# Performance work log

Measured on AMD Instinct MI355X. Metric: run time of the kernel, lower is better.

## Reference

```python
import jax, jax.numpy as jnp
import numpy as np

D_MODEL = 1024
N_HEADS = 16
D_K = D_MODEL // N_HEADS


def setup_inputs() -> dict:
    key = jax.random.key(0)
    ks = jax.random.split(key, 12)
    B, S = 4, 2048
    sc = 1.0 / np.sqrt(D_MODEL)
    inp = {
        "query": jax.random.normal(ks[0], (B, S, D_MODEL), jnp.float32),
        "key": jax.random.normal(ks[1], (B, S, D_MODEL), jnp.float32),
        "value": jax.random.normal(ks[2], (B, S, D_MODEL), jnp.float32),
        "Wq": jax.random.normal(ks[3], (D_MODEL, D_MODEL), jnp.float32) * sc,
        "bq": jnp.zeros((D_MODEL,), jnp.float32),
        "Wk": jax.random.normal(ks[4], (D_MODEL, D_MODEL), jnp.float32) * sc,
        "bk": jnp.zeros((D_MODEL,), jnp.float32),
        "Wv": jax.random.normal(ks[5], (D_MODEL, D_MODEL), jnp.float32) * sc,
        "bv": jnp.zeros((D_MODEL,), jnp.float32),
        "Wo": jax.random.normal(ks[6], (D_MODEL, D_MODEL), jnp.float32) * sc,
        "bo": jnp.zeros((D_MODEL,), jnp.float32),
    }
    return inp


def _split_heads(x):
    B, S, _ = x.shape
    return x.reshape(B, S, N_HEADS, D_K).transpose(0, 2, 1, 3)  # [B,H,S,Dk]


def reference(query, key, value, Wq, bq, Wk, bk, Wv, bv, Wo, bo):
    q = _split_heads(query @ Wq.T + bq)
    k = _split_heads(key @ Wk.T + bk)
    v = _split_heads(value @ Wv.T + bv)
    scores = jnp.einsum("bhqd,bhkd->bhqk", q, k) / jnp.sqrt(jnp.float32(D_K))
    # Faithful to source: softmax over dim=1 (the HEAD axis), a quirk of the original.
    probs = jax.nn.softmax(scores, axis=1)
    attn = jnp.einsum("bhqk,bhkd->bhqd", probs, v)
    B, H, S, Dk = attn.shape
    combined = attn.transpose(0, 2, 1, 3).reshape(B, S, H * Dk)
    return combined @ Wo.T + bo
```

## Files before the change

### kernel.cpp

```cpp
#include <hip/hip_runtime.h>
#include <stdint.h>

typedef __attribute__((ext_vector_type(8))) short bf16x8;
typedef __attribute__((ext_vector_type(4))) float f32x4;
typedef __attribute__((ext_vector_type(4))) float fl4;
typedef __attribute__((ext_vector_type(4))) unsigned short u16x4;
typedef __attribute__((ext_vector_type(8))) unsigned short u16x8;

constexpr int SEQ = 2048;
constexpr int DMODEL = 1024;
constexpr int NH = 16;
constexpr int DKH = 64;
constexpr float SEXP = 0.18033688f;

__device__ __forceinline__ unsigned short f2bf(float x) {
  union { float f; uint32_t u; } c;
  c.f = x;
  uint32_t u = c.u;
  u += 0x7FFFu + ((u >> 16) & 1u);
  return (unsigned short)(u >> 16);
}

__device__ __forceinline__ float bf2f(unsigned short u) {
  union { uint32_t u; float f; } c;
  c.u = ((uint32_t)u) << 16;
  return c.f;
}

__device__ __forceinline__ uint32_t cvtpk(float lo, float hi) {
  uint32_t r;
  asm("v_cvt_pk_bf16_f32 %0, %1, %2" : "=v"(r) : "v"(lo), "v"(hi));
  return r;
}

#if __has_builtin(__builtin_amdgcn_exp2f)
__device__ __forceinline__ float fexp2(float x) { return __builtin_amdgcn_exp2f(x); }
#else
__device__ __forceinline__ float fexp2(float x) { return exp2f(x); }
#endif

__device__ __forceinline__ int swz(int row) { return (row & 3) ^ ((row >> 2) & 3); }

__device__ __forceinline__ void gload16(const unsigned short* g, unsigned short* l) {
  __builtin_amdgcn_global_load_lds((const __attribute__((address_space(1))) void*)g,
                                   (__attribute__((address_space(3))) void*)l, 16, 0, 0);
}

__global__ __launch_bounds__(256) void cvtk(
    const float* __restrict__ s0, const float* __restrict__ s1, const float* __restrict__ s2,
    unsigned short* __restrict__ d0, unsigned short* __restrict__ d1, unsigned short* __restrict__ d2) {
  const float* s = blockIdx.y == 0 ? s0 : blockIdx.y == 1 ? s1 : s2;
  unsigned short* d = blockIdx.y == 0 ? d0 : blockIdx.y == 1 ? d1 : d2;
  const size_t i = ((size_t)blockIdx.x * 256 + threadIdx.x) * 8;
  fl4 a = *(const fl4*)(s + i);
  fl4 c = *(const fl4*)(s + i + 4);
  u16x8 r;
#pragma unroll
  for (int j = 0; j < 4; ++j) { r[j] = f2bf(a[j]); r[4 + j] = f2bf(c[j]); }
  *(u16x8*)(d + i) = r;
}

__global__ __launch_bounds__(256) void cvt1(
    const float* __restrict__ s, unsigned short* __restrict__ d) {
  const size_t i = ((size_t)blockIdx.x * 256 + threadIdx.x) * 8;
  fl4 a = *(const fl4*)(s + i);
  fl4 c = *(const fl4*)(s + i + 4);
  u16x8 r;
#pragma unroll
  for (int j = 0; j < 4; ++j) { r[j] = f2bf(a[j]); r[4 + j] = f2bf(c[j]); }
  *(u16x8*)(d + i) = r;
}

__global__ __launch_bounds__(256, 2) void gemmqkv(
    const float* __restrict__ Xq, const float* __restrict__ Xk, const float* __restrict__ Xv,
    const unsigned short* __restrict__ Wb,
    const float* __restrict__ bq, const float* __restrict__ bk, const float* __restrict__ bv,
    unsigned short* __restrict__ Qp, unsigned short* __restrict__ Kp, unsigned short* __restrict__ Vt) {
  constexpr int K = DMODEL;
  __shared__ unsigned short As[2][128 * 32];
  __shared__ unsigned short Bs[2][128 * 32];
  const int tid = threadIdx.x;
  const int wave = tid >> 6, lane = tid & 63;
  const int g = lane >> 4, ln = lane & 15;
  const int o = blockIdx.x;
  const int x = o & 7, j = o >> 3;
  const int si = j >> 5, w = j & 31;
  const int seg = si >> 1;
  const int r0 = (x * 8 + (si & 1) * 4 + (w & 3)) * 128;
  const int c0 = (w >> 2) * 128;
  const int wr = (wave >> 1) * 64, wc = (wave & 1) * 64;
  const int arow = tid >> 2, cc = tid & 3;

  const float* A = seg == 0 ? Xq : seg == 1 ? Xk : Xv;
  const unsigned short* Bw = Wb + (size_t)seg * DMODEL * DMODEL;
  const float* bias = seg == 0 ? bq : seg == 1 ? bk : bv;
  const float ascale = seg == 0 ? SEXP : 1.0f;

  f32x4 acc[4][4] = {};
  fl4 ar[2][2];

  auto LOADA = [&](int kt) {
#pragma unroll
    for (int i = 0; i < 2; ++i) {
      const size_t ao = (size_t)(r0 + arow + i * 64) * K + kt + cc * 8;
      ar[i][0] = *(const fl4*)(A + ao);
      ar[i][1] = *(const fl4*)(A + ao + 4);
    }
  };
  auto WRITEA = [&](int buf) {
#pragma unroll
    for (int i = 0; i < 2; ++i) {
      const int row = arow + i * 64;
      const int ch = (cc ^ swz(row)) * 8;
      union { uint32_t u[4]; u16x8 v; } pk;
      pk.u[0] = cvtpk(ar[i][0][0], ar[i][0][1]);
      pk.u[1] = cvtpk(ar[i][0][2], ar[i][0][3]);
      pk.u[2] = cvtpk(ar[i][1][0], ar[i][1][1]);
      pk.u[3] = cvtpk(ar[i][1][2], ar[i][1][3]);
      *(u16x8*)(As[buf] + row * 32 + ch) = pk.v;
    }
  };
  auto STAGEB = [&](int buf, int kt) {
#pragma unroll
    for (int i = 0; i < 2; ++i) {
      const int row = i * 64 + (tid >> 2);
      const int cs = ((tid & 3) ^ swz(row)) * 8;
      gload16(Bw + (size_t)(c0 + row) * K + kt + cs, Bs[buf] + (i * 256 + wave * 64) * 8);
    }
  };

  LOADA(0);
  WRITEA(0);
  STAGEB(0, 0);
  __syncthreads();

  for (int t = 0; t < K / 32; ++t) {
    const int buf = t & 1;
    if (t + 1 < K / 32) { LOADA((t + 1) * 32); STAGEB(buf ^ 1, (t + 1) * 32); }
    bf16x8 af[4], bfr[4];
#pragma unroll
    for (int m = 0; m < 4; ++m) {
      const int row = wr + m * 16 + ln;
      af[m] = *(const bf16x8*)(As[buf] + row * 32 + ((g ^ swz(row)) * 8));
    }
#pragma unroll
    for (int n = 0; n < 4; ++n) {
      const int row = wc + n * 16 + ln;
      bfr[n] = *(const bf16x8*)(Bs[buf] + row * 32 + ((g ^ swz(row)) * 8));
    }
#pragma unroll
    for (int m = 0; m < 4; ++m)
#pragma unroll
      for (int n = 0; n < 4; ++n)
        acc[m][n] = __builtin_amdgcn_mfma_f32_16x16x32_bf16(af[m], bfr[n], acc[m][n], 0, 0, 0);
    if (t + 1 < K / 32) WRITEA(buf ^ 1);
    __syncthreads();
  }

#pragma unroll
  for (int m = 0; m < 4; ++m) {
    const int row = r0 + wr + m * 16 + g * 4;
#pragma unroll
    for (int n = 0; n < 4; ++n) {
      const int col = c0 + wc + n * 16 + ln;
      const float bvv = bias[col];
      f32x4 v = acc[m][n];
      if (seg < 2) {
        unsigned short* C = seg == 0 ? Qp : Kp;
#pragma unroll
        for (int r = 0; r < 4; ++r) C[(size_t)(row + r) * DMODEL + col] = f2bf((v[r] + bvv) * ascale);
      } else {
        const int bb = row >> 11, sl = row & 2047;
        const int h = col >> 6, d = col & 63;
        const int sp = (sl & ~31) | (((sl >> 2) & 3) << 3) | (((sl >> 4) & 1) << 2);
        u16x4 pk;
#pragma unroll
        for (int r = 0; r < 4; ++r) pk[r] = f2bf(v[r] + bvv);
        *(u16x4*)(Vt + ((size_t)((bb * NH + h) * DKH + d)) * SEQ + sp) = pk;
      }
    }
  }
}

__global__ __launch_bounds__(256, 2) void gemmout(
    const unsigned short* __restrict__ A, const unsigned short* __restrict__ Bb,
    const float* __restrict__ bias, float* __restrict__ Cp) {
  constexpr int K = DMODEL;
  constexpr int N = DMODEL;
  __shared__ unsigned short As[2][128 * 32];
  __shared__ unsigned short Bs[2][128 * 32];
  const int tid = threadIdx.x;
  const int wave = tid >> 6, lane = tid & 63;
  const int g = lane >> 4, ln = lane & 15;
  const int o = blockIdx.x;
  const int x = o & 7, idx = o >> 3;
  const int r0 = (x * 8 + (idx & 7)) * 128;
  const int c0 = (idx >> 3) * 128;
  const int wr = (wave >> 1) * 64, wc = (wave & 1) * 64;

  f32x4 acc[4][4] = {};

  auto STAGE = [&](int buf, int kt) {
#pragma unroll
    for (int i = 0; i < 2; ++i) {
      const int row = i * 64 + (tid >> 2);
      const int cs = ((tid & 3) ^ swz(row)) * 8;
      gload16(A + (size_t)(r0 + row) * K + kt + cs, As[buf] + (i * 256 + wave * 64) * 8);
      gload16(Bb + (size_t)(c0 + row) * K + kt + cs, Bs[buf] + (i * 256 + wave * 64) * 8);
    }
  };

  STAGE(0, 0);
  __syncthreads();

  for (int t = 0; t < K / 32; ++t) {
    const int buf = t & 1;
    if (t + 1 < K / 32) STAGE(buf ^ 1, (t + 1) * 32);
    bf16x8 af[4], bfr[4];
#pragma unroll
    for (int m = 0; m < 4; ++m) {
      const int row = wr + m * 16 + ln;
      af[m] = *(const bf16x8*)(As[buf] + row * 32 + ((g ^ swz(row)) * 8));
    }
#pragma unroll
    for (int n = 0; n < 4; ++n) {
      const int row = wc + n * 16 + ln;
      bfr[n] = *(const bf16x8*)(Bs[buf] + row * 32 + ((g ^ swz(row)) * 8));
    }
#pragma unroll
    for (int m = 0; m < 4; ++m)
#pragma unroll
      for (int n = 0; n < 4; ++n)
        acc[m][n] = __builtin_amdgcn_mfma_f32_16x16x32_bf16(af[m], bfr[n], acc[m][n], 0, 0, 0);
    __syncthreads();
  }

#pragma unroll
  for (int m = 0; m < 4; ++m) {
    const int row = r0 + wr + m * 16 + g * 4;
#pragma unroll
    for (int n = 0; n < 4; ++n) {
      const int col = c0 + wc + n * 16 + ln;
      const float bvv = bias[col];
      f32x4 v = acc[m][n];
#pragma unroll
      for (int r = 0; r < 4; ++r) Cp[(size_t)(row + r) * N + col] = v[r] + bvv;
    }
  }
}

__global__ __launch_bounds__(256, 3) void denomk(
    const unsigned short* __restrict__ Qp, const unsigned short* __restrict__ Kp,
    unsigned short* __restrict__ rDb) {
  __shared__ unsigned short Ks[2][128 * 64];
  const int tid = threadIdx.x, wave = tid >> 6, lane = tid & 63;
  const int g = lane >> 4, ln = lane & 15;
  const int o = blockIdx.x;
  const int l = (o & 7) * 256 + (o >> 3);
  const int b = l >> 9;
  const int qg = (l >> 4) & 31;
  const int kvg = l & 15;
  const int q0 = qg * 64, kvb = kvg * 128;
  const int kw = wave * 32;

  auto STAGE = [&](int buf, int h) {
#pragma unroll
    for (int i = 0; i < 4; ++i) {
      const int s = i * 256 + tid;
      const int row = s >> 3, c = s & 7;
      gload16(Kp + (size_t)(b * SEQ + kvb + row) * DMODEL + h * DKH + ((c ^ (row & 7)) * 8),
              Ks[buf] + (i * 256 + wave * 64) * 8);
    }
  };

  f32x4 psum[2][4] = {};

  STAGE(0, 0);
  __syncthreads();

  for (int h = 0; h < NH; ++h) {
    const int buf = h & 1;
    if (h + 1 < NH) STAGE(buf ^ 1, h + 1);
    bf16x8 qf[2][4];
#pragma unroll
    for (int ks = 0; ks < 2; ++ks)
#pragma unroll
      for (int n = 0; n < 4; ++n)
        qf[ks][n] = *(const bf16x8*)(Qp + (size_t)(b * SEQ + q0 + n * 16 + ln) * DMODEL + h * DKH + ks * 32 + g * 8);
    bf16x8 kf[2][2];
#pragma unroll
    for (int m = 0; m < 2; ++m)
#pragma unroll
      for (int ks = 0; ks < 2; ++ks) {
        const int r = kw + m * 16 + ln;
        const int cc = ks * 4 + g;
        kf[m][ks] = *(const bf16x8*)(Ks[buf] + r * 64 + ((cc ^ (r & 7)) * 8));
      }
    f32x4 s[2][4] = {};
#pragma unroll
    for (int m = 0; m < 2; ++m)
#pragma unroll
      for (int n = 0; n < 4; ++n) {
        s[m][n] = __builtin_amdgcn_mfma_f32_16x16x32_bf16(kf[m][0], qf[0][n], s[m][n], 0, 0, 0);
        s[m][n] = __builtin_amdgcn_mfma_f32_16x16x32_bf16(kf[m][1], qf[1][n], s[m][n], 0, 0, 0);
      }
#pragma unroll
    for (int m = 0; m < 2; ++m)
#pragma unroll
      for (int n = 0; n < 4; ++n)
#pragma unroll
        for (int r = 0; r < 4; ++r) psum[m][n][r] += fexp2(s[m][n][r]);
    __syncthreads();
  }

#pragma unroll
  for (int m = 0; m < 2; ++m)
#pragma unroll
    for (int n = 0; n < 4; ++n) {
      u16x4 st;
#pragma unroll
      for (int r = 0; r < 4; ++r) st[r] = f2bf(1.0f / psum[m][n][r]);
      *(u16x4*)(rDb + (size_t)(b * SEQ + q0 + n * 16 + ln) * SEQ + kvb + kw + m * 16 + g * 4) = st;
    }
}

__global__ __launch_bounds__(256, 4) void flashk(
    const unsigned short* __restrict__ Qp, const unsigned short* __restrict__ Kp,
    const unsigned short* __restrict__ Vt, const unsigned short* __restrict__ rDb,
    unsigned short* __restrict__ Ab) {
  __shared__ unsigned short Ks[2][64 * 64];
  __shared__ unsigned short Vs[2][64 * 64];
  const int tid = threadIdx.x, wave = tid >> 6, lane = tid & 63;
  const int g = lane >> 4, ln = lane & 15;
  const int o = blockIdx.x;
  const int l = (o & 7) * 128 + (o >> 3);
  const int b = l >> 8;
  const int h = (l >> 4) & 15;
  const int q0 = (l & 15) * 128 + wave * 32;

  bf16x8 qf[2][2];
#pragma unroll
  for (int ks = 0; ks < 2; ++ks)
#pragma unroll
    for (int n = 0; n < 2; ++n)
      qf[ks][n] = *(const bf16x8*)(Qp + (size_t)(b * SEQ + q0 + n * 16 + ln) * DMODEL + h * DKH + ks * 32 + g * 8);

  f32x4 ao[4][2] = {};
  const size_t rbase0 = (size_t)(b * SEQ + q0 + ln) * SEQ;
  const size_t kbase = (size_t)(b * SEQ) * DMODEL + h * DKH;
  const size_t vbase = (size_t)((b * NH + h) * DKH) * SEQ;

  auto STAGE = [&](int buf, int kv0) {
#pragma unroll
    for (int i = 0; i < 2; ++i) {
      const int s = i * 256 + tid;
      const int row = s >> 3, c = s & 7;
      gload16(Kp + kbase + (size_t)(kv0 + row) * DMODEL + ((c ^ (row & 7)) * 8),
              Ks[buf] + (i * 256 + wave * 64) * 8);
    }
#pragma unroll
    for (int i = 0; i < 2; ++i) {
      const int s = i * 256 + tid;
      const int row = s >> 3, c = s & 7;
      gload16(Vt + vbase + (size_t)row * SEQ + kv0 + ((c ^ (row & 7)) * 8),
              Vs[buf] + (i * 256 + wave * 64) * 8);
    }
  };

  STAGE(0, 0);
  __syncthreads();

  for (int t = 0; t < SEQ / 64; ++t) {
    const int kv0 = t * 64, buf = t & 1;
    if (t + 1 < SEQ / 64) STAGE(buf ^ 1, kv0 + 64);

#pragma unroll
    for (int si = 0; si < 2; ++si) {
      u16x4 rdq[2][2];
#pragma unroll
      for (int n = 0; n < 2; ++n)
#pragma unroll
        for (int m = 0; m < 2; ++m)
          rdq[n][m] = *(const u16x4*)(rDb + rbase0 + (size_t)(n * 16) * SEQ + kv0 + si * 32 + m * 16 + g * 4);

      f32x4 s2[2][2] = {};
      __builtin_amdgcn_s_setprio(1);
#pragma unroll
      for (int m = 0; m < 2; ++m) {
        const int row = si * 32 + m * 16 + ln;
#pragma unroll
        for (int ks = 0; ks < 2; ++ks) {
          const int cc = ks * 4 + g;
          bf16x8 kf = *(const bf16x8*)(Ks[buf] + row * 64 + ((cc ^ (row & 7)) * 8));
#pragma unroll
          for (int n = 0; n < 2; ++n)
            s2[m][n] = __builtin_amdgcn_mfma_f32_16x16x32_bf16(kf, qf[ks][n], s2[m][n], 0, 0, 0);
        }
      }
      __builtin_amdgcn_s_setprio(0);

      bf16x8 pfr[2];
#pragma unroll
      for (int n = 0; n < 2; ++n) {
        uint32_t dw[4];
#pragma unroll
        for (int m = 0; m < 2; ++m) {
          float p0 = fexp2(s2[m][n][0]) * bf2f(rdq[n][m][0]);
          float p1 = fexp2(s2[m][n][1]) * bf2f(rdq[n][m][1]);
          float p2 = fexp2(s2[m][n][2]) * bf2f(rdq[n][m][2]);
          float p3 = fexp2(s2[m][n][3]) * bf2f(rdq[n][m][3]);
          dw[m * 2 + 0] = cvtpk(p0, p1);
          dw[m * 2 + 1] = cvtpk(p2, p3);
        }
        union { uint32_t u[4]; bf16x8 v; } cv;
        cv.u[0] = dw[0]; cv.u[1] = dw[1]; cv.u[2] = dw[2]; cv.u[3] = dw[3];
        pfr[n] = cv.v;
      }

      __builtin_amdgcn_s_setprio(1);
#pragma unroll
      for (int dt = 0; dt < 4; ++dt) {
        const int vrow = dt * 16 + ln;
        const int vc = si * 4 + g;
        bf16x8 vf = *(const bf16x8*)(Vs[buf] + vrow * 64 + ((vc ^ (vrow & 7)) * 8));
#pragma unroll
        for (int n = 0; n < 2; ++n)
          ao[dt][n] = __builtin_amdgcn_mfma_f32_16x16x32_bf16(vf, pfr[n], ao[dt][n], 0, 0, 0);
      }
      __builtin_amdgcn_s_setprio(0);
    }
    __syncthreads();
  }

#pragma unroll
  for (int dt = 0; dt < 4; ++dt)
#pragma unroll
    for (int n = 0; n < 2; ++n) {
      u16x4 st;
#pragma unroll
      for (int r = 0; r < 4; ++r) st[r] = f2bf(ao[dt][n][r]);
      *(u16x4*)(Ab + (size_t)(b * SEQ + q0 + n * 16 + ln) * DMODEL + h * DKH + dt * 16 + g * 4) = st;
    }
}

extern "C" void kernel_launch(void* const* d_in, const int* in_sizes, int n_in,
                              void* d_out, int out_size, void* d_ws, size_t ws_size,
                              hipStream_t stream) {
  (void)in_sizes; (void)n_in; (void)out_size; (void)ws_size;
  const float* query = (const float*)d_in[0];
  const float* key   = (const float*)d_in[1];
  const float* value = (const float*)d_in[2];
  const float* Wq = (const float*)d_in[3];
  const float* bq = (const float*)d_in[4];
  const float* Wk = (const float*)d_in[5];
  const float* bk = (const float*)d_in[6];
  const float* Wv = (const float*)d_in[7];
  const float* bv = (const float*)d_in[8];
  const float* Wo = (const float*)d_in[9];
  const float* bo = (const float*)d_in[10];

  uint8_t* ws = (uint8_t*)d_ws;
  const size_t SZ = (size_t)4 * SEQ * DMODEL * 2;
  const size_t WSZ = (size_t)DMODEL * DMODEL;
  unsigned short* Qp  = (unsigned short*)(ws);
  unsigned short* Wob = (unsigned short*)(ws);
  unsigned short* Kp  = (unsigned short*)(ws + SZ);
  unsigned short* Vt  = (unsigned short*)(ws + 2 * SZ);
  unsigned short* Wqb = (unsigned short*)(ws + 3 * SZ);
  unsigned short* Wkb = Wqb + WSZ;
  unsigned short* Wvb = Wqb + 2 * WSZ;
  unsigned short* Ab  = (unsigned short*)(ws + 3 * SZ);
  unsigned short* rDb = (unsigned short*)d_out;

  cvtk<<<dim3(512, 3), 256, 0, stream>>>(Wq, Wk, Wv, Wqb, Wkb, Wvb);
  gemmqkv<<<1536, 256, 0, stream>>>(query, key, value, Wqb, bq, bk, bv, Qp, Kp, Vt);
  denomk<<<2048, 256, 0, stream>>>(Qp, Kp, rDb);
  flashk<<<1024, 256, 0, stream>>>(Qp, Kp, Vt, rDb, Ab);
  cvt1<<<512, 256, 0, stream>>>(Wo, Wob);
  gemmout<<<512, 256, 0, stream>>>(Ab, Wob, bo, (float*)d_out);
}
```

Measured before the change: 388.6 us.

## Replace __syncthreads with explicit vmcnt waits to keep prefetch loads in flight

All four main kernels (QKV projection, output projection, denominator, attention) replace __syncthreads with raw s_barrier plus partial s_waitcnt vmcnt counts, using sched_barrier to fix instruction order. The next tile's loads stay outstanding while the current tile is computed, removing the full memory drain that __syncthreads forces. Loop-tail prefetches are made unconditional with wrapped indices, and the attention kernel hoists both halves of the rDb loads before the barrier. The risk is hand-counted vmcnt values that must exactly match the number of issued loads, plus a redundant extra prefetch on the last iteration.

```diff
diff --git a/kernel.cpp b/kernel.cpp
--- a/kernel.cpp
+++ b/kernel.cpp
@@ -45,6 +45,11 @@
   __builtin_amdgcn_global_load_lds((const __attribute__((address_space(1))) void*)g,
                                    (__attribute__((address_space(3))) void*)l, 16, 0, 0);
 }
+
+#define SB() __builtin_amdgcn_sched_barrier(0)
+#define VW(N) do { SB(); asm volatile("s_waitcnt vmcnt(" #N ")" ::: "memory"); SB(); } while (0)
+#define LGKM0() do { SB(); asm volatile("s_waitcnt lgkmcnt(0)" ::: "memory"); SB(); } while (0)
+__device__ __forceinline__ void bar() { SB(); __builtin_amdgcn_s_barrier(); SB(); }
 
 __global__ __launch_bounds__(256) void cvtk(
     const float* __restrict__ s0, const float* __restrict__ s1, const float* __restrict__ s2,
@@ -128,34 +133,45 @@
       gload16(Bw + (size_t)(c0 + row) * K + kt + cs, Bs[buf] + (i * 256 + wave * 64) * 8);
     }
   };
+  auto COMPUTE = [&](int buf) {
+    bf16x8 af[4], bfr[4];
+#pragma unroll
+    for (int m = 0; m < 4; ++m) {
+      const int row = wr + m * 16 + ln;
+      af[m] = *(const bf16x8*)(As[buf] + row * 32 + ((g ^ swz(row)) * 8));
+    }
+#pragma unroll
+    for (int n = 0; n < 4; ++n) {
+      const int row = wc + n * 16 + ln;
+      bfr[n] = *(const bf16x8*)(Bs[buf] + row * 32 + ((g ^ swz(row)) * 8));
+    }
+#pragma unroll
+    for (int m = 0; m < 4; ++m)
+#pragma unroll
+      for (int n = 0; n < 4; ++n)
+        acc[m][n] = __builtin_amdgcn_mfma_f32_16x16x32_bf16(af[m], bfr[n], acc[m][n], 0, 0, 0);
+  };
 
   LOADA(0);
   WRITEA(0);
   STAGEB(0, 0);
-  __syncthreads();
+  LGKM0();
+  bar();
 
   for (int t = 0; t < K / 32; ++t) {
     const int buf = t & 1;
-    if (t + 1 < K / 32) { LOADA((t + 1) * 32); STAGEB(buf ^ 1, (t + 1) * 32); }
-    bf16x8 af[4], bfr[4];
-#pragma unroll
-    for (int m = 0; m < 4; ++m) {
-      const int row = wr + m * 16 + ln;
-      af[m] = *(const bf16x8*)(As[buf] + row * 32 + ((g ^ swz(row)) * 8));
-    }
-#pragma unroll
-    for (int n = 0; n < 4; ++n) {
-      const int row = wc + n * 16 + ln;
-      bfr[n] = *(const bf16x8*)(Bs[buf] + row * 32 + ((g ^ swz(row)) * 8));
-    }
-#pragma unroll
-    for (int m = 0; m < 4; ++m)
-#pragma unroll
-      for (int n = 0; n < 4; ++n)
-        acc[m][n] = __builtin_amdgcn_mfma_f32_16x16x32_bf16(af[m], bfr[n], acc[m][n], 0, 0, 0);
-    if (t + 1 < K / 32) WRITEA(buf ^ 1);
-    __syncthreads();
+    const int ktn = ((t + 1) & 31) * 32;
+    STAGEB(buf ^ 1, ktn);
+    SB();
+    LOADA(ktn);
+    VW(6);
+    bar();
+    COMPUTE(buf);
+    WRITEA(buf ^ 1);
+    LGKM0();
+    bar();
   }
+  VW(0);
 
 #pragma unroll
   for (int m = 0; m < 4; ++m) {
@@ -211,11 +227,12 @@
   };
 
   STAGE(0, 0);
-  __syncthreads();
 
   for (int t = 0; t < K / 32; ++t) {
     const int buf = t & 1;
-    if (t + 1 < K / 32) STAGE(buf ^ 1, (t + 1) * 32);
+    STAGE(buf ^ 1, ((t + 1) & 31) * 32);
+    VW(4);
+    bar();
     bf16x8 af[4], bfr[4];
 #pragma unroll
     for (int m = 0; m < 4; ++m) {
@@ -232,8 +249,9 @@
 #pragma unroll
       for (int n = 0; n < 4; ++n)
         acc[m][n] = __builtin_amdgcn_mfma_f32_16x16x32_bf16(af[m], bfr[n], acc[m][n], 0, 0, 0);
-    __syncthreads();
+    bar();
   }
+  VW(0);
 
 #pragma unroll
   for (int m = 0; m < 4; ++m) {
@@ -276,17 +294,19 @@
   f32x4 psum[2][4] = {};
 
   STAGE(0, 0);
-  __syncthreads();
 
   for (int h = 0; h < NH; ++h) {
     const int buf = h & 1;
-    if (h + 1 < NH) STAGE(buf ^ 1, h + 1);
+    STAGE(buf ^ 1, (h + 1) & 15);
+    SB();
     bf16x8 qf[2][4];
 #pragma unroll
     for (int ks = 0; ks < 2; ++ks)
 #pragma unroll
       for (int n = 0; n < 4; ++n)
         qf[ks][n] = *(const bf16x8*)(Qp + (size_t)(b * SEQ + q0 + n * 16 + ln) * DMODEL + h * DKH + ks * 32 + g * 8);
+    VW(12);
+    bar();
     bf16x8 kf[2][2];
 #pragma unroll
     for (int m = 0; m < 2; ++m)
@@ -310,8 +330,9 @@
       for (int n = 0; n < 4; ++n)
 #pragma unroll
         for (int r = 0; r < 4; ++r) psum[m][n][r] += fexp2(s[m][n][r]);
-    __syncthreads();
+    bar();
   }
+  VW(0);
 
 #pragma unroll
   for (int m = 0; m < 2; ++m)
@@ -368,21 +389,24 @@
   };
 
   STAGE(0, 0);
-  __syncthreads();
 
   for (int t = 0; t < SEQ / 64; ++t) {
     const int kv0 = t * 64, buf = t & 1;
-    if (t + 1 < SEQ / 64) STAGE(buf ^ 1, kv0 + 64);
+    STAGE(buf ^ 1, (kv0 + 64) & (SEQ - 1));
+    SB();
+    u16x4 rdq[2][2][2];
+#pragma unroll
+    for (int s2 = 0; s2 < 2; ++s2)
+#pragma unroll
+      for (int n = 0; n < 2; ++n)
+#pragma unroll
+        for (int m = 0; m < 2; ++m)
+          rdq[s2][n][m] = *(const u16x4*)(rDb + rbase0 + (size_t)(n * 16) * SEQ + kv0 + s2 * 32 + m * 16 + g * 4);
+    VW(12);
+    bar();
 
 #pragma unroll
     for (int si = 0; si < 2; ++si) {
-      u16x4 rdq[2][2];
-#pragma unroll
-      for (int n = 0; n < 2; ++n)
-#pragma unroll
-        for (int m = 0; m < 2; ++m)
-          rdq[n][m] = *(const u16x4*)(rDb + rbase0 + (size_t)(n * 16) * SEQ + kv0 + si * 32 + m * 16 + g * 4);
-
       f32x4 s2[2][2] = {};
       __builtin_amdgcn_s_setprio(1);
 #pragma unroll
@@ -405,10 +429,10 @@
         uint32_t dw[4];
 #pragma unroll
         for (int m = 0; m < 2; ++m) {
-          float p0 = fexp2(s2[m][n][0]) * bf2f(rdq[n][m][0]);
-          float p1 = fexp2(s2[m][n][1]) * bf2f(rdq[n][m][1]);
-          float p2 = fexp2(s2[m][n][2]) * bf2f(rdq[n][m][2]);
-          float p3 = fexp2(s2[m][n][3]) * bf2f(rdq[n][m][3]);
+          float p0 = fexp2(s2[m][n][0]) * bf2f(rdq[si][n][m][0]);
+          float p1 = fexp2(s2[m][n][1]) * bf2f(rdq[si][n][m][1]);
+          float p2 = fexp2(s2[m][n][2]) * bf2f(rdq[si][n][m][2]);
+          float p3 = fexp2(s2[m][n][3]) * bf2f(rdq[si][n][m][3]);
           dw[m * 2 + 0] = cvtpk(p0, p1);
           dw[m * 2 + 1] = cvtpk(p2, p3);
         }
@@ -429,8 +453,9 @@
       }
       __builtin_amdgcn_s_setprio(0);
     }
-    __syncthreads();
+    bar();
   }
+  VW(0);
 
 #pragma unroll
   for (int dt = 0; dt < 4; ++dt)
```

After: 392.1 us. Within noise of the previous version (+0.9%).
